# Optimization experiments

Hardware: AMD Instinct MI355X
Metric: run time of the kernel (lower is better)

Reference implementation:

```python
import jax, jax.numpy as jnp
import numpy as np

B, S, E, NH = 2, 2048, 1024, 8
DH = E // NH


def setup_inputs() -> dict:
    key = jax.random.key(0)
    ks = jax.random.split(key, 8)
    q = jax.random.normal(ks[0], (B, S, E), dtype=jnp.float32)
    k = jax.random.normal(ks[1], (B, S, E), dtype=jnp.float32)
    v = jax.random.normal(ks[2], (B, S, E), dtype=jnp.float32)
    # gate projections: Linear(3E -> NH)
    igate_w = jax.random.normal(ks[3], (NH, 3 * E), dtype=jnp.float32) * 0.02
    igate_b = jax.random.normal(ks[4], (NH,), dtype=jnp.float32) * 0.1
    fgate_w = jax.random.normal(ks[5], (NH, 3 * E), dtype=jnp.float32) * 0.02
    fgate_b = jnp.linspace(3.0, 6.0, NH, dtype=jnp.float32)  # bias_linspace_init_
    norm_weight = 1.0 + 0.01 * jax.random.normal(ks[6], (E,), dtype=jnp.float32)
    return {"q": q, "k": k, "v": v, "igate_w": igate_w, "igate_b": igate_b,
            "fgate_w": fgate_w, "fgate_b": fgate_b, "norm_weight": norm_weight}


def _mlstm_forward(q, k, v, igate_w, igate_b, fgate_w, fgate_b, norm_weight):
    eps = 1e-6
    gate_in = jnp.concatenate([q, k, v], axis=-1)            # (B,S,3E)
    i_pre = gate_in @ igate_w.T + igate_b                    # (B,S,NH)
    f_pre = gate_in @ fgate_w.T + fgate_b                    # (B,S,NH)
    i_pre = jnp.transpose(i_pre, (0, 2, 1))                  # (B,NH,S)
    f_pre = jnp.transpose(f_pre, (0, 2, 1))                  # (B,NH,S)

    qh = jnp.transpose(q.reshape(B, S, NH, DH), (0, 2, 1, 3))  # (B,NH,S,DH)
    kh = jnp.transpose(k.reshape(B, S, NH, DH), (0, 2, 1, 3))
    vh = jnp.transpose(v.reshape(B, S, NH, DH), (0, 2, 1, 3))

    # cumulative log forget gates; decay matrix D[i,j] = sum_{u=j+1..i} logsig(f_u) + i_pre[j]
    log_fg = jax.nn.log_sigmoid(f_pre)                       # (B,NH,S)
    cs = jnp.cumsum(log_fg, axis=-1)                         # (B,NH,S)
    diff = cs[:, :, :, None] - cs[:, :, None, :]             # (B,NH,S,S) = cs[i]-cs[j]
    causal = jnp.tril(jnp.ones((S, S), dtype=bool))
    log_fg_mat = jnp.where(causal, diff, -jnp.inf)
    log_D = log_fg_mat + i_pre[:, :, None, :]                # (B,NH,S,S)

    max_log_D = jnp.max(log_D, axis=-1, keepdims=True)       # rowwise stabilizer
    D = jnp.exp(log_D - max_log_D)

    qk = jnp.einsum("bhsd,bhtd->bhst", qh, kh / jnp.sqrt(jnp.float32(DH)))
    C = qk * D
    normalizer = jnp.maximum(jnp.abs(jnp.sum(C, axis=-1, keepdims=True)),
                             jnp.exp(-max_log_D))
    Cn = C / (normalizer + eps)
    h = jnp.einsum("bhst,bhtd->bhsd", Cn, vh)                # (B,NH,S,DH)

    # MultiHeadLayerNorm == group_norm(num_groups=NH): per-head, per-token over DH
    mu = jnp.mean(h, axis=-1, keepdims=True)
    var = jnp.var(h, axis=-1, keepdims=True)
    hn = (h - mu) / jnp.sqrt(var + 1e-5)
    hn = hn * norm_weight.reshape(NH, DH)[None, :, None, :]
    return jnp.transpose(hn, (0, 2, 1, 3)).reshape(B, S, E)


def reference(q, k, v, igate_w, igate_b, fgate_w, fgate_b, norm_weight):
    return _mlstm_forward(q, k, v, igate_w, igate_b, fgate_w, fgate_b, norm_weight)
```

## Files before the change

kernel.cpp:

```cpp
#include <hip/hip_runtime.h>
#include <hip/hip_bf16.h>
#include <math.h>

typedef __attribute__((ext_vector_type(8))) short bf16x8;
typedef __attribute__((ext_vector_type(16))) float f32x16;

namespace {
constexpr int kB = 2, kS = 2048, kE = 1024, kNH = 8, kDH = 128, kE3 = 3072;
constexpr float kLog2e = 1.4426950408889634f;
constexpr int kUnits = 27;
constexpr int kSplitPerBh = 20;
}

__device__ const int kOrder[kUnits] = {6,19,20,17,18,5,15,16,13,14,24,25,4,
                                       11,12,21,22,23,26,9,10,3,7,8,2,1,0};

__device__ __forceinline__ ushort f2bf(float x) {
  union { __hip_bfloat16 b; ushort u; } c; c.b = __float2bfloat16(x); return c.u;
}
__device__ __forceinline__ uint pk2(float a, float b) {
  return (uint)f2bf(a) | ((uint)f2bf(b) << 16);
}
__device__ __forceinline__ void gload16(const void* g, void* l) {
  __builtin_amdgcn_global_load_lds(
      (const __attribute__((address_space(1))) void*)g,
      (__attribute__((address_space(3))) void*)l, 16, 0, 0);
}
__device__ __forceinline__ f32x16 zero16() {
  f32x16 z;
#pragma unroll
  for (int i = 0; i < 16; ++i) z[i] = 0.f;
  return z;
}
union UB8 { uint4 u; bf16x8 f; };

__device__ __forceinline__ float butterfly64(float* acc, int lane) {
#define BF_LEVEL(BMASK, HALF)                                          \
  {                                                                    \
    const bool hib = (lane & (BMASK)) != 0;                            \
    _Pragma("unroll")                                                  \
    for (int i = 0; i < (HALF); ++i) {                                 \
      const float keep = hib ? acc[i + (HALF)] : acc[i];               \
      const float send = hib ? acc[i] : acc[i + (HALF)];               \
      acc[i] = keep + __shfl_xor(send, (BMASK));                       \
    }                                                                  \
  }
  BF_LEVEL(1, 32)
  BF_LEVEL(2, 16)
  BF_LEVEL(4, 8)
  BF_LEVEL(8, 4)
  BF_LEVEL(16, 2)
  BF_LEVEL(32, 1)
#undef BF_LEVEL
  return acc[0];
}

__global__ __launch_bounds__(256, 2) void prep_kernel(
    const float* __restrict__ q, const float* __restrict__ k, const float* __restrict__ v,
    const float* __restrict__ iw, const float* __restrict__ ib,
    const float* __restrict__ fw, const float* __restrict__ fb,
    ushort* __restrict__ Kb, ushort* __restrict__ Vtb,
    float* __restrict__ gtmp) {
  const int bid = blockIdx.x;
  const int tid = threadIdx.x;
  __shared__ ushort Vst[128 * 128];
  __shared__ float red[4][64];

  if (bid < 256) {
    const int bh = bid >> 4;
    const int b = bh >> 3, h = bh & 7;
    const int s0 = (bid & 15) * 128;
#pragma unroll
    for (int iter = 0; iter < 4; ++iter) {
      const int tl = iter * 32 + (tid >> 3);
      const int d0 = (tid & 7) * 16;
      const int s = s0 + tl;
      const size_t base = ((size_t)b * kS + s) * kE + h * kDH + d0;
      const float4 k0 = *reinterpret_cast<const float4*>(k + base);
      const float4 k1 = *reinterpret_cast<const float4*>(k + base + 4);
      const float4 k2 = *reinterpret_cast<const float4*>(k + base + 8);
      const float4 k3 = *reinterpret_cast<const float4*>(k + base + 12);
      uint4 pa, pb;
      pa.x = pk2(k0.x, k0.y); pa.y = pk2(k0.z, k0.w);
      pa.z = pk2(k1.x, k1.y); pa.w = pk2(k1.z, k1.w);
      pb.x = pk2(k2.x, k2.y); pb.y = pk2(k2.z, k2.w);
      pb.z = pk2(k3.x, k3.y); pb.w = pk2(k3.z, k3.w);
      ushort* kd = Kb + ((size_t)bh * kS + s) * 128 + d0;
      *reinterpret_cast<uint4*>(kd) = pa;
      *reinterpret_cast<uint4*>(kd + 8) = pb;

      const float4 v0 = *reinterpret_cast<const float4*>(v + base);
      const float4 v1 = *reinterpret_cast<const float4*>(v + base + 4);
      const float4 v2 = *reinterpret_cast<const float4*>(v + base + 8);
      const float4 v3 = *reinterpret_cast<const float4*>(v + base + 12);
      uint4 va, vb4;
      va.x = pk2(v0.x, v0.y); va.y = pk2(v0.z, v0.w);
      va.z = pk2(v1.x, v1.y); va.w = pk2(v1.z, v1.w);
      vb4.x = pk2(v2.x, v2.y); vb4.y = pk2(v2.z, v2.w);
      vb4.z = pk2(v3.x, v3.y); vb4.w = pk2(v3.z, v3.w);
      const int c0 = d0 >> 3;
      char* row = reinterpret_cast<char*>(Vst) + tl * 256;
      *reinterpret_cast<uint4*>(row + (((c0 + 0) ^ (tl & 15)) << 4)) = va;
      *reinterpret_cast<uint4*>(row + (((c0 + 1) ^ (tl & 15)) << 4)) = vb4;
    }
    __syncthreads();
    {
      const int d = tid >> 1, half = tid & 1;
      const int cd = d >> 3;
      const int od = (d & 7) * 2;
      uint tmp[32];
#pragma unroll
      for (int p = 0; p < 32; ++p) {
        const int t = half * 64 + 2 * p;
        const ushort u0 = *reinterpret_cast<const ushort*>(
            reinterpret_cast<const char*>(Vst) + t * 256 + ((cd ^ (t & 15)) << 4) + od);
        const ushort u1 = *reinterpret_cast<const ushort*>(
            reinterpret_cast<const char*>(Vst) + (t + 1) * 256 + ((cd ^ ((t + 1) & 15)) << 4) + od);
        tmp[p] = (uint)u0 | ((uint)u1 << 16);
      }
      ushort* vd = Vtb + ((size_t)bh * kDH + d) * kS + s0 + half * 64;
#pragma unroll
      for (int p = 0; p < 8; ++p)
        *reinterpret_cast<uint4*>(vd + p * 8) = *reinterpret_cast<const uint4*>(&tmp[p * 4]);
    }
  } else {
    const int w = tid >> 6, lane = tid & 63;
    const int tokbase = (bid - 256) * 4;
    float acc[64];
#pragma unroll
    for (int i = 0; i < 64; ++i) acc[i] = 0.f;

    for (int step = 0; step < 12; ++step) {
      const int e = w * 768 + step * 64 + lane;
      const int seg = e >> 10;
      const int eo = e & 1023;
      const float* __restrict__ src = (seg == 0) ? q : (seg == 1) ? k : v;
      float gv[4];
#pragma unroll
      for (int t = 0; t < 4; ++t)
        gv[t] = src[(size_t)(tokbase + t) * kE + eo];
      float w4[4];
#pragma unroll
      for (int hh = 0; hh < 4; ++hh) w4[hh] = iw[hh * kE3 + e];
#pragma unroll
      for (int t = 0; t < 4; ++t)
#pragma unroll
        for (int hh = 0; hh < 4; ++hh)
          acc[t * 16 + hh] += gv[t] * w4[hh];
#pragma unroll
      for (int hh = 0; hh < 4; ++hh) w4[hh] = iw[(4 + hh) * kE3 + e];
#pragma unroll
      for (int t = 0; t < 4; ++t)
#pragma unroll
        for (int hh = 0; hh < 4; ++hh)
          acc[t * 16 + 4 + hh] += gv[t] * w4[hh];
#pragma unroll
      for (int hh = 0; hh < 4; ++hh) w4[hh] = fw[hh * kE3 + e];
#pragma unroll
      for (int t = 0; t < 4; ++t)
#pragma unroll
        for (int hh = 0; hh < 4; ++hh)
          acc[t * 16 + 8 + hh] += gv[t] * w4[hh];
#pragma unroll
      for (int hh = 0; hh < 4; ++hh) w4[hh] = fw[(4 + hh) * kE3 + e];
#pragma unroll
      for (int t = 0; t < 4; ++t)
#pragma unroll
        for (int hh = 0; hh < 4; ++hh)
          acc[t * 16 + 12 + hh] += gv[t] * w4[hh];
    }
    const float r = butterfly64(acc, lane);
    const int a = ((lane & 1) << 5) | ((lane & 2) << 3) | ((lane & 4) << 1) |
                  ((lane & 8) >> 1) | ((lane & 16) >> 3) | ((lane & 32) >> 5);
    red[w][a] = r;
    __syncthreads();
    if (tid < 64) {
      const float val = red[0][tid] + red[1][tid] + red[2][tid] + red[3][tid];
      const int t = tid >> 4, gate = tid & 15, hh = gate & 7;
      gtmp[(size_t)(tokbase + t) * 16 + gate] =
          val + (gate < 8 ? ib[hh] : fb[hh]);
    }
  }
}

__global__ __launch_bounds__(256) void scan_kernel(
    const float* __restrict__ gtmp,
    float* __restrict__ wt_out, float* __restrict__ M2_out, float* __restrict__ nfl_out,
    float* __restrict__ Cg) {
  const int bh = blockIdx.x;
  const int b = bh >> 3, h = bh & 7;
  const int tid = threadIdx.x;
  const int w = tid >> 6, lane = tid & 63;
  __shared__ float wsum[4], wmax[4];
  const float* __restrict__ gt = gtmp + (size_t)b * kS * 16;
  const int s0 = tid * 8;

  float lf[8];
#pragma unroll
  for (int j = 0; j < 8; ++j) {
    const float f = gt[(size_t)(s0 + j) * 16 + 8 + h];
    lf[j] = fminf(f, 0.f) - log1pf(expf(-fabsf(f)));
  }
  float run = 0.f, pcs[8];
#pragma unroll
  for (int j = 0; j < 8; ++j) { run += lf[j]; pcs[j] = run; }
  float x = run;
#pragma unroll
  for (int d = 1; d < 64; d <<= 1) {
    const float t = __shfl_up(x, d);
    if (lane >= d) x += t;
  }
  if (lane == 63) wsum[w] = x;
  __syncthreads();
  float woff = 0.f;
#pragma unroll
  for (int i = 0; i < 4; ++i) if (i < w) woff += wsum[i];
  const float csbase = woff + x - run;
  float cs[8];
#pragma unroll
  for (int j = 0; j < 8; ++j) cs[j] = csbase + pcs[j];

  float av[8];
#pragma unroll
  for (int j = 0; j < 8; ++j)
    av[j] = gt[(size_t)(s0 + j) * 16 + h] - cs[j];
  float rmax = -1e30f, pm[8];
#pragma unroll
  for (int j = 0; j < 8; ++j) { rmax = fmaxf(rmax, av[j]); pm[j] = rmax; }

  float tm = rmax;
  tm = fmaxf(tm, __shfl_xor(tm, 1));
  tm = fmaxf(tm, __shfl_xor(tm, 2));
  tm = fmaxf(tm, __shfl_xor(tm, 4));
  if ((lane & 7) == 0) Cg[bh * 32 + (tid >> 3)] = tm * kLog2e;

  float4 wtlo, wthi;
  wtlo.x = exp2f((av[0] - tm) * kLog2e); wtlo.y = exp2f((av[1] - tm) * kLog2e);
  wtlo.z = exp2f((av[2] - tm) * kLog2e); wtlo.w = exp2f((av[3] - tm) * kLog2e);
  wthi.x = exp2f((av[4] - tm) * kLog2e); wthi.y = exp2f((av[5] - tm) * kLog2e);
  wthi.z = exp2f((av[6] - tm) * kLog2e); wthi.w = exp2f((av[7] - tm) * kLog2e);

  float mi = rmax;
#pragma unroll
  for (int d = 1; d < 64; d <<= 1) {
    const float t = __shfl_up(mi, d);
    if (lane >= d) mi = fmaxf(mi, t);
  }
  if (lane == 63) wmax[w] = mi;
  float mexcl = __shfl_up(mi, 1);
  if (lane == 0) mexcl = -1e30f;
  __syncthreads();
  float wmoff = -1e30f;
#pragma unroll
  for (int i = 0; i < 4; ++i) if (i < w) wmoff = fmaxf(wmoff, wmax[i]);
  const float mbase = fmaxf(wmoff, mexcl);

  float M[8];
#pragma unroll
  for (int j = 0; j < 8; ++j) M[j] = fmaxf(mbase, pm[j]);
  float4 m2lo, m2hi, nflo, nfhi;
  m2lo.x = M[0] * kLog2e; m2lo.y = M[1] * kLog2e; m2lo.z = M[2] * kLog2e; m2lo.w = M[3] * kLog2e;
  m2hi.x = M[4] * kLog2e; m2hi.y = M[5] * kLog2e; m2hi.z = M[6] * kLog2e; m2hi.w = M[7] * kLog2e;
  nflo.x = expf(-(cs[0] + M[0])); nflo.y = expf(-(cs[1] + M[1]));
  nflo.z = expf(-(cs[2] + M[2])); nflo.w = expf(-(cs[3] + M[3]));
  nfhi.x = expf(-(cs[4] + M[4])); nfhi.y = expf(-(cs[5] + M[5]));
  nfhi.z = expf(-(cs[6] + M[6])); nfhi.w = expf(-(cs[7] + M[7]));
  const size_t o = (size_t)bh * kS + s0;
  *reinterpret_cast<float4*>(wt_out + o) = wtlo;
  *reinterpret_cast<float4*>(wt_out + o + 4) = wthi;
  *reinterpret_cast<float4*>(M2_out + o) = m2lo;
  *reinterpret_cast<float4*>(M2_out + o + 4) = m2hi;
  *reinterpret_cast<float4*>(nfl_out + o) = nflo;
  *reinterpret_cast<float4*>(nfl_out + o + 4) = nfhi;
}

__global__ __launch_bounds__(256, 2) void attn_mfma_kernel(
    const float* __restrict__ qg, const ushort* __restrict__ Kb,
    const ushort* __restrict__ Vtb, const float* __restrict__ wt,
    const float* __restrict__ Cg, const float* __restrict__ M2,
    const float* __restrict__ nfl, const float* __restrict__ nw,
    float* __restrict__ out, float* __restrict__ ph, float* __restrict__ prs) {
  const int id = blockIdx.x;
  const int r8 = id & 7, qq = id >> 3;
  const int bh = r8 + 8 * (qq & 1);
  const int u = kOrder[qq >> 1];
  const int b = bh >> 3, h = bh & 7;
  int it, j0, j1, cid = -1;
  if (u <= 6) { it = u; const int T = 2 * it + 2; j0 = 0; j1 = T - 1; }
  else if (u <= 20) {
    const int s = u - 7; it = 7 + (s >> 1); const int ci = s & 1;
    const int T = 2 * it + 2;
    j0 = (T * ci) >> 1; j1 = ((T * (ci + 1)) >> 1) - 1;
    cid = bh * kSplitPerBh + (u - 7);
  } else {
    const int s = u - 21; it = 14 + (s >= 3 ? 1 : 0); const int ci = s - (s >= 3 ? 3 : 0);
    const int T = 2 * it + 2;
    j0 = (T * ci) / 3; j1 = (T * (ci + 1)) / 3 - 1;
    cid = bh * kSplitPerBh + (u - 7);
  }
  const int tid = threadIdx.x;
  const int w = tid >> 6, lane = tid & 63;
  const int l31 = lane & 31, hi = lane >> 5;
  const int row_w = it * 128 + w * 32;
  const int ig = row_w + l31;
  const size_t bhS = (size_t)bh * kS;

  __shared__ ushort Klds[64 * 128];
  __shared__ ushort Vlds[128 * 64];
  __shared__ float Wtl[64];

  const char* __restrict__ KgBase = reinterpret_cast<const char*>(Kb + bhS * 128);
  const char* __restrict__ VgBase = reinterpret_cast<const char*>(Vtb + (size_t)bh * 128 * kS);
  const char* __restrict__ WgBase = reinterpret_cast<const char*>(wt + bhS);

  bf16x8 qf[8];
  {
    const float scale = 0.08838834764831845f;
    const float* qrow = qg + ((size_t)b * kS + ig) * kE + h * kDH;
#pragma unroll
    for (int ks = 0; ks < 8; ++ks) {
      const int d0 = ks * 16 + hi * 8;
      const float4 lo = *reinterpret_cast<const float4*>(qrow + d0);
      const float4 hi4 = *reinterpret_cast<const float4*>(qrow + d0 + 4);
      UB8 f;
      f.u.x = pk2(lo.x * scale, lo.y * scale);
      f.u.y = pk2(lo.z * scale, lo.w * scale);
      f.u.z = pk2(hi4.x * scale, hi4.y * scale);
      f.u.w = pk2(hi4.z * scale, hi4.w * scale);
      qf[ks] = f.f;
    }
  }
  const float M2i = M2[bhS + ig];
  const float cgreg = Cg[bh * 32 + l31];

  int koffG[4], voffG[4];
#pragma unroll
  for (int i = 0; i < 4; ++i) {
    const int L = tid * 16 + i * 4096;
    { const int j = L >> 8, c = (L >> 4) & 15;
      koffG[i] = j * 256 + ((c ^ (j & 15)) << 4); }
    { const int d = L >> 7, c = (L >> 4) & 7;
      voffG[i] = d * 4096 + ((c ^ (d & 7)) << 4); }
  }
  auto stage = [&](int jt) {
    const char* Kg = KgBase + (size_t)jt * 16384;
    const char* Vg = VgBase + (size_t)jt * 128;
    char* kl = reinterpret_cast<char*>(Klds) + tid * 16;
    char* vl = reinterpret_cast<char*>(Vlds) + tid * 16;
#pragma unroll
    for (int i = 0; i < 4; ++i) gload16(Kg + koffG[i], kl + i * 4096);
#pragma unroll
    for (int i = 0; i < 4; ++i) gload16(Vg + voffG[i], vl + i * 4096);
    if (tid < 16)
      gload16(WgBase + jt * 256 + tid * 16,
              reinterpret_cast<char*>(Wtl) + tid * 16);
  };

  f32x16 hacc[4];
#pragma unroll
  for (int dc = 0; dc < 4; ++dc) hacc[dc] = zero16();
  float rs = 0.f;

  for (int jt = j0; jt <= j1; ++jt) {
    __syncthreads();
    stage(jt);
    __syncthreads();

    const int jlo = jt * 64;
    const bool v0 = (jlo <= row_w + 31);
    const bool v1 = (jlo + 32 <= row_w + 31);
    const bool fullmask = (jlo + 63 <= row_w);
    if (!v0) continue;

    const float f = exp2f(__shfl(cgreg, jt) - M2i);
    const char* kb = reinterpret_cast<const char*>(Klds);
    const char* vb = reinterpret_cast<const char*>(Vlds);
    const int ksw = (l31 & 15) << 4;

    f32x16 sacc0 = zero16(), sacc1 = zero16();
#pragma unroll
    for (int ks = 0; ks < 8; ++ks) {
      const int colb = 32 * ks + 16 * hi;
      const bf16x8 kf0 = *reinterpret_cast<const bf16x8*>(
          kb + l31 * 256 + (colb ^ ksw));
      sacc0 = __builtin_amdgcn_mfma_f32_32x32x16_bf16(kf0, qf[ks], sacc0, 0, 0, 0);
      if (v1) {
        const bf16x8 kf1 = *reinterpret_cast<const bf16x8*>(
            kb + (32 + l31) * 256 + (colb ^ ksw));
        sacc1 = __builtin_amdgcn_mfma_f32_32x32x16_bf16(kf1, qf[ks], sacc1, 0, 0, 0);
      }
    }

    uint pkw[2][8];
#pragma unroll
    for (int jc = 0; jc < 2; ++jc) {
      if (jc == 1 && !v1) break;
      const f32x16 sa = jc ? sacc1 : sacc0;
      float p[16];
#pragma unroll
      for (int q2 = 0; q2 < 4; ++q2) {
        const float4 wq = *reinterpret_cast<const float4*>(
            &Wtl[jc * 32 + q2 * 8 + 4 * hi]);
        const float wv[4] = {wq.x, wq.y, wq.z, wq.w};
#pragma unroll
        for (int m = 0; m < 4; ++m) {
          const int r = q2 * 4 + m;
          const int c = m + 8 * q2;
          float val = sa[r] * (wv[m] * f);
          if (!fullmask) val = (jlo + jc * 32 + c + 4 * hi <= ig) ? val : 0.f;
          rs += val; p[r] = val;
        }
      }
#pragma unroll
      for (int q2 = 0; q2 < 8; ++q2) pkw[jc][q2] = pk2(p[2 * q2], p[2 * q2 + 1]);
    }

#pragma unroll
    for (int ks = 0; ks < 4; ++ks) {
      const int jc = ks >> 1, ks2 = ks & 1;
      if (jc == 1 && !v1) break;
      UB8 pf;
      pf.u.x = pkw[jc][ks2 * 4 + 0]; pf.u.y = pkw[jc][ks2 * 4 + 1];
      pf.u.z = pkw[jc][ks2 * 4 + 2]; pf.u.w = pkw[jc][ks2 * 4 + 3];
      const int colb = 64 * jc + 32 * ks2 + 8 * hi;
#pragma unroll
      for (int dc = 0; dc < 4; ++dc) {
        const int d = dc * 32 + l31;
        const char* vrow = vb + d * 128;
        const int sw = (d & 7) << 4;
        const uint2 a = *reinterpret_cast<const uint2*>(vrow + (colb ^ sw));
        const uint2 c = *reinterpret_cast<const uint2*>(vrow + ((colb + 16) ^ sw));
        UB8 vf; vf.u.x = a.x; vf.u.y = a.y; vf.u.z = c.x; vf.u.w = c.y;
        hacc[dc] = __builtin_amdgcn_mfma_f32_32x32x16_bf16(pf.f, vf.f, hacc[dc], 0, 0, 0);
      }
    }
  }

  const float rs_tot = rs + __shfl_xor(rs, 32);

  if (cid >= 0) {
    float* pb = ph + (size_t)cid * 16384;
#pragma unroll
    for (int dc = 0; dc < 4; ++dc)
#pragma unroll
      for (int r = 0; r < 16; ++r) {
        const int il = w * 32 + (r & 3) + 8 * (r >> 2) + 4 * hi;
        pb[il * 128 + dc * 32 + l31] = hacc[dc][r];
      }
    if (hi == 0) prs[cid * 128 + w * 32 + l31] = rs_tot;
    return;
  }

  float nwv[4];
#pragma unroll
  for (int dc = 0; dc < 4; ++dc) nwv[dc] = nw[h * kDH + dc * 32 + l31];
#pragma unroll
  for (int r = 0; r < 16; ++r) {
    const int imap = (r & 3) + 8 * (r >> 2) + 4 * hi;
    const float rsum = __shfl(rs_tot, imap);
    const float nf = nfl[bhS + row_w + imap];
    const float inv = 1.f / (fmaxf(fabsf(rsum), nf) + 1e-6f);
    float hv[4];
    float s1 = 0.f, s2 = 0.f;
#pragma unroll
    for (int dc = 0; dc < 4; ++dc) {
      hv[dc] = hacc[dc][r] * inv;
      s1 += hv[dc]; s2 += hv[dc] * hv[dc];
    }
#pragma unroll
    for (int off = 1; off <= 16; off <<= 1) {
      s1 += __shfl_xor(s1, off);
      s2 += __shfl_xor(s2, off);
    }
    const float mu = s1 * (1.f / 128.f);
    const float var = s2 * (1.f / 128.f) - mu * mu;
    const float rstd = rsqrtf(var + 1e-5f);
    float* __restrict__ orow = out + ((size_t)b * kS + row_w + imap) * kE + h * kDH;
#pragma unroll
    for (int dc = 0; dc < 4; ++dc)
      orow[dc * 32 + l31] = (hv[dc] - mu) * rstd * nwv[dc];
  }
}

__global__ __launch_bounds__(256) void combine_kernel(
    const float* __restrict__ ph, const float* __restrict__ prs,
    const float* __restrict__ nfl, const float* __restrict__ nw,
    float* __restrict__ out) {
  const int blk = blockIdx.x;
  const int bh = blk / 9, ct = blk % 9;
  const int b = bh >> 3, h = bh & 7;
  const int it = 7 + ct;
  const int nc = (ct < 7) ? 2 : 3;
  const int cb0 = bh * kSplitPerBh + ((ct < 7) ? ct * 2 : 14 + (ct - 7) * 3);
  const int tid = threadIdx.x;
  __shared__ float sinv[128];
  if (tid < 128) {
    float rsum = 0.f;
    for (int c = 0; c < nc; ++c) rsum += prs[(cb0 + c) * 128 + tid];
    const float nf = nfl[(size_t)bh * kS + it * 128 + tid];
    sinv[tid] = 1.f / (fmaxf(fabsf(rsum), nf) + 1e-6f);
  }
  __syncthreads();
  for (int kk = 0; kk < 16; ++kk) {
    const int idx = kk * 256 + tid;
    const int row = idx >> 5, c4 = idx & 31;
    float ax = 0.f, ay = 0.f, az = 0.f, aw = 0.f;
    for (int c = 0; c < nc; ++c) {
      const float4 t = *reinterpret_cast<const float4*>(
          ph + (size_t)(cb0 + c) * 16384 + row * 128 + c4 * 4);
      ax += t.x; ay += t.y; az += t.z; aw += t.w;
    }
    const float inv = sinv[row];
    ax *= inv; ay *= inv; az *= inv; aw *= inv;
    float s1 = ax + ay + az + aw;
    float s2 = ax * ax + ay * ay + az * az + aw * aw;
#pragma unroll
    for (int off = 1; off <= 16; off <<= 1) {
      s1 += __shfl_xor(s1, off);
      s2 += __shfl_xor(s2, off);
    }
    const float mu = s1 * (1.f / 128.f);
    const float var = s2 * (1.f / 128.f) - mu * mu;
    const float rstd = rsqrtf(var + 1e-5f);
    const float4 nw4 = *reinterpret_cast<const float4*>(nw + h * kDH + c4 * 4);
    float4 o;
    o.x = (ax - mu) * rstd * nw4.x;
    o.y = (ay - mu) * rstd * nw4.y;
    o.z = (az - mu) * rstd * nw4.z;
    o.w = (aw - mu) * rstd * nw4.w;
    *reinterpret_cast<float4*>(
        out + ((size_t)b * kS + it * 128 + row) * kE + h * kDH + c4 * 4) = o;
  }
}

extern "C" void kernel_launch(void* const* d_in, const int* in_sizes, int n_in,
                              void* d_out, int out_size, void* d_ws, size_t ws_size,
                              hipStream_t stream) {
  const float* q  = (const float*)d_in[0];
  const float* k  = (const float*)d_in[1];
  const float* v  = (const float*)d_in[2];
  const float* iw = (const float*)d_in[3];
  const float* ib = (const float*)d_in[4];
  const float* fw = (const float*)d_in[5];
  const float* fb = (const float*)d_in[6];
  const float* nw = (const float*)d_in[7];
  float* out = (float*)d_out;

  char* ws = (char*)d_ws;
  const int BHS = kB * kNH * kS;
  float* gtmp  = (float*)ws;
  float* wt    = gtmp + 2 * BHS;
  float* M2    = gtmp + 3 * BHS;
  float* nfl   = gtmp + 4 * BHS;
  float* Cg    = gtmp + 5 * BHS;
  ushort* Kb  = (ushort*)(ws + (size_t)(5 * BHS + 512) * 4);
  ushort* Vtb = Kb + (size_t)kB * kNH * kS * kDH;
  float* ph   = (float*)(Vtb + (size_t)kB * kNH * kS * kDH);
  float* prs  = ph + (size_t)320 * 128 * 128;

  prep_kernel<<<dim3(1280), dim3(256), 0, stream>>>(q, k, v, iw, ib, fw, fb,
                                                    Kb, Vtb, gtmp);
  scan_kernel<<<dim3(kB * kNH), dim3(256), 0, stream>>>(gtmp, wt, M2, nfl, Cg);
  attn_mfma_kernel<<<dim3(kUnits * kB * kNH), dim3(256), 0, stream>>>(
      q, Kb, Vtb, wt, Cg, M2, nfl, nw, out, ph, prs);
  combine_kernel<<<dim3(kB * kNH * 9), dim3(256), 0, stream>>>(ph, prs, nfl, nw, out);
}
```

Before: 100.5 us.

## Double-buffer K/V/W tiles in LDS to overlap global loads with MFMA

Allocates two LDS buffers for the K, V and gate-weight tiles and prefetches the next tile with async global-to-LDS loads while the current tile is computed. Explicit vmcnt waits and raw s_barriers with sched barriers replace the two __syncthreads per iteration. Every wave now issues the weight-tile load so that vmcnt counts match across waves. The cost is doubled LDS use, which may lower occupancy, plus redundant weight-tile loads.

```diff
diff --git a/kernel.cpp b/kernel.cpp
--- a/kernel.cpp
+++ b/kernel.cpp
@@ -305,9 +305,9 @@
   const int ig = row_w + l31;
   const size_t bhS = (size_t)bh * kS;
 
-  __shared__ ushort Klds[64 * 128];
-  __shared__ ushort Vlds[128 * 64];
-  __shared__ float Wtl[64];
+  __shared__ ushort Klds[2 * 64 * 128];
+  __shared__ ushort Vlds[2 * 128 * 64];
+  __shared__ float Wtl[2 * 64];
 
   const char* __restrict__ KgBase = reinterpret_cast<const char*>(Kb + bhS * 128);
   const char* __restrict__ VgBase = reinterpret_cast<const char*>(Vtb + (size_t)bh * 128 * kS);
@@ -332,6 +332,8 @@
   }
   const float M2i = M2[bhS + ig];
   const float cgreg = Cg[bh * 32 + l31];
+  asm volatile("" : : "v"(M2i), "v"(cgreg));
+  asm volatile("s_waitcnt vmcnt(0)" ::: "memory");
 
   int koffG[4], voffG[4];
 #pragma unroll
@@ -342,18 +344,18 @@
     { const int d = L >> 7, c = (L >> 4) & 7;
       voffG[i] = d * 4096 + ((c ^ (d & 7)) << 4); }
   }
-  auto stage = [&](int jt) {
+  auto stage = [&](int buf, int jt) {
     const char* Kg = KgBase + (size_t)jt * 16384;
     const char* Vg = VgBase + (size_t)jt * 128;
-    char* kl = reinterpret_cast<char*>(Klds) + tid * 16;
-    char* vl = reinterpret_cast<char*>(Vlds) + tid * 16;
+    char* kl = reinterpret_cast<char*>(Klds) + buf * 16384 + tid * 16;
+    char* vl = reinterpret_cast<char*>(Vlds) + buf * 16384 + tid * 16;
 #pragma unroll
     for (int i = 0; i < 4; ++i) gload16(Kg + koffG[i], kl + i * 4096);
 #pragma unroll
     for (int i = 0; i < 4; ++i) gload16(Vg + voffG[i], vl + i * 4096);
-    if (tid < 16)
-      gload16(WgBase + jt * 256 + tid * 16,
-              reinterpret_cast<char*>(Wtl) + tid * 16);
+    if (lane < 16)
+      gload16(WgBase + jt * 256 + lane * 16,
+              reinterpret_cast<char*>(Wtl) + buf * 256 + lane * 16);
   };
 
   f32x16 hacc[4];
@@ -361,79 +363,92 @@
   for (int dc = 0; dc < 4; ++dc) hacc[dc] = zero16();
   float rs = 0.f;
 
+  stage(0, j0);
+
   for (int jt = j0; jt <= j1; ++jt) {
-    __syncthreads();
-    stage(jt);
-    __syncthreads();
+    const int cur = (jt - j0) & 1;
+    if (jt < j1) {
+      stage(cur ^ 1, jt + 1);
+      asm volatile("s_waitcnt vmcnt(9)" ::: "memory");
+    } else {
+      asm volatile("s_waitcnt vmcnt(0)" ::: "memory");
+    }
+    __builtin_amdgcn_sched_barrier(0);
+    __builtin_amdgcn_s_barrier();
+    __builtin_amdgcn_sched_barrier(0);
 
     const int jlo = jt * 64;
     const bool v0 = (jlo <= row_w + 31);
     const bool v1 = (jlo + 32 <= row_w + 31);
     const bool fullmask = (jlo + 63 <= row_w);
-    if (!v0) continue;
-
-    const float f = exp2f(__shfl(cgreg, jt) - M2i);
-    const char* kb = reinterpret_cast<const char*>(Klds);
-    const char* vb = reinterpret_cast<const char*>(Vlds);
-    const int ksw = (l31 & 15) << 4;
-
-    f32x16 sacc0 = zero16(), sacc1 = zero16();
-#pragma unroll
-    for (int ks = 0; ks < 8; ++ks) {
-      const int colb = 32 * ks + 16 * hi;
-      const bf16x8 kf0 = *reinterpret_cast<const bf16x8*>(
-          kb + l31 * 256 + (colb ^ ksw));
-      sacc0 = __builtin_amdgcn_mfma_f32_32x32x16_bf16(kf0, qf[ks], sacc0, 0, 0, 0);
-      if (v1) {
-        const bf16x8 kf1 = *reinterpret_cast<const bf16x8*>(
-            kb + (32 + l31) * 256 + (colb ^ ksw));
-        sacc1 = __builtin_amdgcn_mfma_f32_32x32x16_bf16(kf1, qf[ks], sacc1, 0, 0, 0);
-      }
-    }
-
-    uint pkw[2][8];
-#pragma unroll
-    for (int jc = 0; jc < 2; ++jc) {
-      if (jc == 1 && !v1) break;
-      const f32x16 sa = jc ? sacc1 : sacc0;
-      float p[16];
-#pragma unroll
-      for (int q2 = 0; q2 < 4; ++q2) {
-        const float4 wq = *reinterpret_cast<const float4*>(
-            &Wtl[jc * 32 + q2 * 8 + 4 * hi]);
-        const float wv[4] = {wq.x, wq.y, wq.z, wq.w};
-#pragma unroll
-        for (int m = 0; m < 4; ++m) {
-          const int r = q2 * 4 + m;
-          const int c = m + 8 * q2;
-          float val = sa[r] * (wv[m] * f);
-          if (!fullmask) val = (jlo + jc * 32 + c + 4 * hi <= ig) ? val : 0.f;
-          rs += val; p[r] = val;
+
+    if (v0) {
+      const float f = exp2f(__shfl(cgreg, jt) - M2i);
+      const char* kb = reinterpret_cast<const char*>(Klds) + cur * 16384;
+      const char* vb = reinterpret_cast<const char*>(Vlds) + cur * 16384;
+      const float* Wf = Wtl + cur * 64;
+      const int ksw = (l31 & 15) << 4;
+
+      f32x16 sacc0 = zero16(), sacc1 = zero16();
+#pragma unroll
+      for (int ks = 0; ks < 8; ++ks) {
+        const int colb = 32 * ks + 16 * hi;
+        const bf16x8 kf0 = *reinterpret_cast<const bf16x8*>(kb + l31 * 256 + (colb ^ ksw));
+        sacc0 = __builtin_amdgcn_mfma_f32_32x32x16_bf16(kf0, qf[ks], sacc0, 0, 0, 0);
+        if (v1) {
+          const bf16x8 kf1 = *reinterpret_cast<const bf16x8*>(
+              kb + (32 + l31) * 256 + (colb ^ ksw));
+          sacc1 = __builtin_amdgcn_mfma_f32_32x32x16_bf16(kf1, qf[ks], sacc1, 0, 0, 0);
         }
       }
-#pragma unroll
-      for (int q2 = 0; q2 < 8; ++q2) pkw[jc][q2] = pk2(p[2 * q2], p[2 * q2 + 1]);
-    }
-
-#pragma unroll
-    for (int ks = 0; ks < 4; ++ks) {
-      const int jc = ks >> 1, ks2 = ks & 1;
-      if (jc == 1 && !v1) break;
-      UB8 pf;
-      pf.u.x = pkw[jc][ks2 * 4 + 0]; pf.u.y = pkw[jc][ks2 * 4 + 1];
-      pf.u.z = pkw[jc][ks2 * 4 + 2]; pf.u.w = pkw[jc][ks2 * 4 + 3];
-      const int colb = 64 * jc + 32 * ks2 + 8 * hi;
-#pragma unroll
-      for (int dc = 0; dc < 4; ++dc) {
-        const int d = dc * 32 + l31;
-        const char* vrow = vb + d * 128;
-        const int sw = (d & 7) << 4;
-        const uint2 a = *reinterpret_cast<const uint2*>(vrow + (colb ^ sw));
-        const uint2 c = *reinterpret_cast<const uint2*>(vrow + ((colb + 16) ^ sw));
-        UB8 vf; vf.u.x = a.x; vf.u.y = a.y; vf.u.z = c.x; vf.u.w = c.y;
-        hacc[dc] = __builtin_amdgcn_mfma_f32_32x32x16_bf16(pf.f, vf.f, hacc[dc], 0, 0, 0);
+
+      uint pkw[2][8];
+#pragma unroll
+      for (int jc = 0; jc < 2; ++jc) {
+        if (jc == 1 && !v1) break;
+        const f32x16 sa = jc ? sacc1 : sacc0;
+        float p[16];
+#pragma unroll
+        for (int q2 = 0; q2 < 4; ++q2) {
+          const float4 wq = *reinterpret_cast<const float4*>(
+              &Wf[jc * 32 + q2 * 8 + 4 * hi]);
+          const float wv[4] = {wq.x, wq.y, wq.z, wq.w};
+#pragma unroll
+          for (int m = 0; m < 4; ++m) {
+            const int r = q2 * 4 + m;
+            const int c = m + 8 * q2;
+            float val = sa[r] * (wv[m] * f);
+            if (!fullmask) val = (jlo + jc * 32 + c + 4 * hi <= ig) ? val : 0.f;
+            rs += val; p[r] = val;
+          }
+        }
+#pragma unroll
+        for (int q2 = 0; q2 < 8; ++q2) pkw[jc][q2] = pk2(p[2 * q2], p[2 * q2 + 1]);
       }
-    }
+
+#pragma unroll
+      for (int ks = 0; ks < 4; ++ks) {
+        const int jc = ks >> 1, ks2 = ks & 1;
+        if (jc == 1 && !v1) break;
+        UB8 pf;
+        pf.u.x = pkw[jc][ks2 * 4 + 0]; pf.u.y = pkw[jc][ks2 * 4 + 1];
+        pf.u.z = pkw[jc][ks2 * 4 + 2]; pf.u.w = pkw[jc][ks2 * 4 + 3];
+        const int colb = 64 * jc + 32 * ks2 + 8 * hi;
+#pragma unroll
+        for (int dc = 0; dc < 4; ++dc) {
+          const int d = dc * 32 + l31;
+          const char* vrow = vb + d * 128;
+          const int sw = (d & 7) << 4;
+          const uint2 a = *reinterpret_cast<const uint2*>(vrow + (colb ^ sw));
+          const uint2 c = *reinterpret_cast<const uint2*>(vrow + ((colb + 16) ^ sw));
+          UB8 vf; vf.u.x = a.x; vf.u.y = a.y; vf.u.z = c.x; vf.u.w = c.y;
+          hacc[dc] = __builtin_amdgcn_mfma_f32_32x32x16_bf16(pf.f, vf.f, hacc[dc], 0, 0, 0);
+        }
+      }
+    }
+    __builtin_amdgcn_sched_barrier(0);
+    __builtin_amdgcn_s_barrier();
+    __builtin_amdgcn_sched_barrier(0);
   }
 
   const float rs_tot = rs + __shfl_xor(rs, 32);
```

Result: no change. 101.8 us (+1.2%).
